# Optimization experiments

Measured on AMD Instinct MI355X. Metric: run time of the kernel, lower is better.

The kernel has to match this reference:

```python
import jax, jax.numpy as jnp
import numpy as np

B, N, D, L = 8, 128, 512, 48
NUM_GCN_LAYERS = 2


def setup_inputs() -> dict:
    key = jax.random.key(0)
    ks = jax.random.split(key, 10)
    gcn_inputs = jax.random.normal(ks[0], (B, N, D), dtype=jnp.float32)
    word_seq_len = jax.random.randint(ks[1], (B,), 1, N + 1)
    adj_matrix = jax.random.randint(ks[2], (B, N, N), 0, 2).astype(jnp.float32)
    dep_label_matrix = jax.random.randint(ks[3], (B, N, N), 0, L)
    # per-label weight matrices, stored (L, out_dim, in_dim) as consumed by the bmm
    w_params = jax.random.normal(ks[4], (L, D, D), dtype=jnp.float32) * 0.05
    mlp_w0 = jax.random.normal(ks[5], (D, D), dtype=jnp.float32) * (1.0 / np.sqrt(D))
    mlp_b0 = jnp.zeros((D,), dtype=jnp.float32)
    mlp_w1 = jax.random.normal(ks[6], (D, D), dtype=jnp.float32) * (1.0 / np.sqrt(D))
    mlp_b1 = jnp.zeros((D,), dtype=jnp.float32)
    return {
        'gcn_inputs': gcn_inputs,
        'word_seq_len': word_seq_len,
        'adj_matrix': adj_matrix,
        'dep_label_matrix': dep_label_matrix,
        'w_params': w_params,
        'mlp_w0': mlp_w0,
        'mlp_b0': mlp_b0,
        'mlp_w1': mlp_w1,
        'mlp_b1': mlp_b1,
    }


def reference(gcn_inputs, word_seq_len, adj_matrix, dep_label_matrix,
              w_params, mlp_w0, mlp_b0, mlp_w1, mlp_b1):
    # denom: in-degree + 1 (self)
    denom = adj_matrix.sum(axis=2, keepdims=True) + 1.0  # (B, N, 1)
    b_idx = jnp.arange(B)[:, None, None]                  # (B,1,1)
    j_idx = jnp.arange(N)[None, None, :]                  # (1,1,N)
    h = gcn_inputs
    for _ in range(NUM_GCN_LAYERS):
        # transform every node by every label matrix: (B, L, N, D)
        t = jnp.einsum('ldk,bjk->bljd', w_params, h)
        # gather per-edge label transform: g[b,i,j,:] = t[b, lab[b,i,j], j, :]
        g = t[b_idx, dep_label_matrix, j_idx]             # (B, N, N, D)
        msg = (adj_matrix[..., None] * g).sum(axis=2)     # (B, N, D)
        h = jax.nn.relu(msg / denom)
    x = jax.nn.relu(h @ mlp_w0.T + mlp_b0)
    x = jax.nn.relu(x @ mlp_w1.T + mlp_b1)
    return x
```

## Files before the change

kernel.cpp:

```cpp
#include <hip/hip_runtime.h>
#include <hip/hip_bf16.h>


typedef unsigned short u16;
typedef unsigned int u32;
using bf16x8 = __bf16 __attribute__((ext_vector_type(8)));
using f32x4 = float __attribute__((ext_vector_type(4)));

__device__ __forceinline__ u16 f2bf(float f) {
  u32 u = __float_as_uint(f);
  u32 r = u + 0x7fffu + ((u >> 16) & 1u);
  return (u16)(r >> 16);
}
__device__ __forceinline__ float bf2f(u16 h) {
  return __uint_as_float(((u32)h) << 16);
}

__device__ __forceinline__ void gl_lds16(const u16* g, u16* l) {
  __builtin_amdgcn_global_load_lds(
      (const __attribute__((address_space(1))) u32*)g,
      (__attribute__((address_space(3))) u32*)l, 16, 0, 0);
}

__global__ __launch_bounds__(256)
void cvt_f32_bf16(const float* __restrict__ in, u16* __restrict__ out, int n4) {
  int stride = gridDim.x * blockDim.x;
  for (int i = blockIdx.x * blockDim.x + threadIdx.x; i < n4; i += stride) {
    float4 v = ((const float4*)in)[i];
    uint2 o;
    o.x = (u32)f2bf(v.x) | ((u32)f2bf(v.y) << 16);
    o.y = (u32)f2bf(v.z) | ((u32)f2bf(v.w) << 16);
    ((uint2*)out)[i] = o;
  }
}

__global__ __launch_bounds__(256)
void prep_mlp_w(const float* __restrict__ w0, const float* __restrict__ w1,
                u16* __restrict__ Bp1, u16* __restrict__ Bp2) {
  int idx = blockIdx.x * 256 + threadIdx.x;
  if (idx < 262144) {
    const int n = idx >> 9, k = idx & 511;
    const float v = w0[idx];
    const u16 hi = f2bf(v);
    const float lo = v - bf2f(hi);
    Bp1[n * 1024 + k] = hi;
    Bp1[n * 1024 + 512 + k] = f2bf(lo);
  } else {
    const int j = idx - 262144;
    const int n = j >> 9, k = j & 511;
    const float v = w1[j];
    const u16 hi = f2bf(v);
    const float lo = v - bf2f(hi);
    Bp2[n * 1536 + k] = hi;
    Bp2[n * 1536 + 512 + k] = f2bf(lo);
    Bp2[n * 1536 + 1024 + k] = hi;
  }
}

#define BM 128
#define BN 128
#define BK 32

template <int MODE>
__global__ __launch_bounds__(256)
void gemm_nt_bf16(const u16* __restrict__ A, const u16* __restrict__ B,
                  void* __restrict__ C, int N, int K, int KC) {
  __shared__ u16 sA[3][BM * BK];
  __shared__ u16 sB[3][BN * BK];
  const int tid = threadIdx.x;
  const int lane = tid & 63;
  const int wid = tid >> 6;
  const int wm = wid >> 1;
  const int wn = wid & 1;

  int m0, n0, kc;
  if (MODE == 0) {
    const int bid = blockIdx.x;
    const int xcd = bid & 7;
    const int r = bid >> 3;
    m0 = (r & 7) * BM;
    n0 = (xcd * 24 + (r >> 3)) * BN;
    kc = 0;
  } else {
    m0 = blockIdx.y * BM;
    n0 = blockIdx.x * BN;
    kc = blockIdx.z;
  }

  const int srow = tid >> 2;
  const int scol = (tid & 3) * 8;
  const u16* gA0 = A + (size_t)(m0 + srow) * K + kc * KC + scol;
  const u16* gA1 = A + (size_t)(m0 + 64 + srow) * K + kc * KC + scol;
  const u16* gB0 = B + (size_t)(n0 + srow) * K + kc * KC + scol;
  const u16* gB1 = B + (size_t)(n0 + 64 + srow) * K + kc * KC + scol;

  auto stage = [&](int buf, int kt) {
    const int ko = kt * BK;
    gl_lds16(gA0 + ko, &sA[buf][tid * 8]);
    gl_lds16(gA1 + ko, &sA[buf][2048 + tid * 8]);
    gl_lds16(gB0 + ko, &sB[buf][tid * 8]);
    gl_lds16(gB1 + ko, &sB[buf][2048 + tid * 8]);
  };

  f32x4 acc[4][4];
#pragma unroll
  for (int i = 0; i < 4; ++i)
#pragma unroll
    for (int j = 0; j < 4; ++j)
      acc[i][j] = (f32x4){0.f, 0.f, 0.f, 0.f};

  const int NT = KC / BK;

  stage(0, 0);
  if (NT > 1) {
    stage(1, 1);
    asm volatile("s_waitcnt vmcnt(4)" ::: "memory");
  } else {
    asm volatile("s_waitcnt vmcnt(0)" ::: "memory");
  }
  __builtin_amdgcn_s_barrier();
  __builtin_amdgcn_sched_barrier(0);

  const int r15 = lane & 15;
  const int ksub = (lane >> 4) * 8;
  for (int kt = 0; kt < NT; ++kt) {
    const int buf = kt % 3;
    if (kt + 2 < NT) stage((kt + 2) % 3, kt + 2);

    bf16x8 af[4], bfr[4];
#pragma unroll
    for (int mi = 0; mi < 4; ++mi)
      af[mi] = *(const bf16x8*)&sA[buf][(wm * 64 + mi * 16 + r15) * BK + ksub];
#pragma unroll
    for (int ni = 0; ni < 4; ++ni)
      bfr[ni] = *(const bf16x8*)&sB[buf][(wn * 64 + ni * 16 + r15) * BK + ksub];

#pragma unroll
    for (int mi = 0; mi < 4; ++mi)
#pragma unroll
      for (int ni = 0; ni < 4; ++ni)
        acc[mi][ni] = __builtin_amdgcn_mfma_f32_16x16x32_bf16(
            af[mi], bfr[ni], acc[mi][ni], 0, 0, 0);

    if (kt + 1 < NT) {
      if (kt + 2 < NT)
        asm volatile("s_waitcnt vmcnt(4)" ::: "memory");
      else
        asm volatile("s_waitcnt vmcnt(0)" ::: "memory");
      __builtin_amdgcn_s_barrier();
      __builtin_amdgcn_sched_barrier(0);
    }
  }

  const int rq = (lane >> 4) * 4;
#pragma unroll
  for (int mi = 0; mi < 4; ++mi) {
#pragma unroll
    for (int ni = 0; ni < 4; ++ni) {
      const int row = m0 + wm * 64 + mi * 16 + rq;
      const int col = n0 + wn * 64 + ni * 16 + r15;
      f32x4 v = acc[mi][ni];
      if (MODE == 0) {
        u16* Cb = (u16*)C;
        const size_t base = (size_t)row * N + col;
#pragma unroll
        for (int r = 0; r < 4; ++r)
          Cb[base + (size_t)r * N] = f2bf(v[r]);
      } else {
        float* Cf = (float*)C + (size_t)kc * 1024 * N;
#pragma unroll
        for (int r = 0; r < 4; ++r)
          Cf[(size_t)(row + r) * N + col] = v[r];
      }
    }
  }
}

template <bool DUP>
__global__ __launch_bounds__(256)
void gcn_agg(const u16* __restrict__ T, const float* __restrict__ adj,
             const int* __restrict__ lab, u16* __restrict__ Hout) {
  const int bid = blockIdx.x;
  const int b = bid & 7;
  const int i = bid >> 3;
  const int bi = b * 128 + i;
  const int tid = threadIdx.x;
  __shared__ float s_adj[128];
  __shared__ int s_off[128];
  if (tid < 128) {
    s_adj[tid] = adj[(size_t)bi * 128 + tid];
    const int lv = lab[(size_t)bi * 128 + tid];
    s_off[tid] = ((b * 128 + tid) * 48 + lv) * 512;
  }
  __syncthreads();

  const int d = tid * 2;
  float den = 1.0f, a0 = 0.f, a1 = 0.f;
#pragma unroll 4
  for (int j = 0; j < 128; ++j) {
    const float a = s_adj[j];
    if (a != 0.0f) {
      den += 1.0f;
      const u32 u = *(const u32*)&T[(size_t)s_off[j] + d];
      a0 += __uint_as_float((u & 0xffffu) << 16);
      a1 += __uint_as_float(u & 0xffff0000u);
    }
  }
  const float r = 1.0f / den;
  a0 = fmaxf(a0 * r, 0.0f);
  a1 = fmaxf(a1 * r, 0.0f);
  const u32 o = (u32)f2bf(a0) | ((u32)f2bf(a1) << 16);
  if (DUP) {
    *(u32*)&Hout[(size_t)bi * 1024 + d] = o;
    *(u32*)&Hout[(size_t)bi * 1024 + 512 + d] = o;
  } else {
    *(u32*)&Hout[(size_t)bi * 512 + d] = o;
  }
}

__global__ __launch_bounds__(256)
void combine_mlp1(const float* __restrict__ P, const float* __restrict__ bias,
                  u16* __restrict__ Ap2) {
  const int idx = blockIdx.x * 256 + threadIdx.x;
  const int m = idx >> 8;
  const int n = (idx & 255) * 2;
  float s0 = 0.f, s1 = 0.f;
#pragma unroll
  for (int s = 0; s < 4; ++s) {
    const float2 v = *(const float2*)&P[(size_t)s * 524288 + m * 512 + n];
    s0 += v.x; s1 += v.y;
  }
  const float x0 = fmaxf(s0 + bias[n], 0.f);
  const float x1 = fmaxf(s1 + bias[n + 1], 0.f);
  const u16 h0 = f2bf(x0), h1 = f2bf(x1);
  const float l0 = x0 - bf2f(h0), l1 = x1 - bf2f(h1);
  const u32 hh = (u32)h0 | ((u32)h1 << 16);
  const u32 ll = (u32)f2bf(l0) | ((u32)f2bf(l1) << 16);
  const size_t base = (size_t)m * 1536 + n;
  *(u32*)&Ap2[base] = hh;
  *(u32*)&Ap2[base + 512] = hh;
  *(u32*)&Ap2[base + 1024] = ll;
}

__global__ __launch_bounds__(256)
void combine_mlp2(const float* __restrict__ P, const float* __restrict__ bias,
                  float* __restrict__ out) {
  const int idx = blockIdx.x * 256 + threadIdx.x;
  const int m = idx >> 7;
  const int n = (idx & 127) * 4;
  float4 s = {0.f, 0.f, 0.f, 0.f};
#pragma unroll
  for (int t = 0; t < 6; ++t) {
    const float4 v = *(const float4*)&P[(size_t)t * 524288 + m * 512 + n];
    s.x += v.x; s.y += v.y; s.z += v.z; s.w += v.w;
  }
  const float4 b = *(const float4*)&bias[n];
  float4 o;
  o.x = fmaxf(s.x + b.x, 0.f);
  o.y = fmaxf(s.y + b.y, 0.f);
  o.z = fmaxf(s.z + b.z, 0.f);
  o.w = fmaxf(s.w + b.w, 0.f);
  *(float4*)&out[(size_t)m * 512 + n] = o;
}

extern "C" void kernel_launch(void* const* d_in, const int* in_sizes, int n_in,
                              void* d_out, int out_size, void* d_ws, size_t ws_size,
                              hipStream_t stream) {
  const float* gcn_inputs = (const float*)d_in[0];
  const float* adj = (const float*)d_in[2];
  const int* lab = (const int*)d_in[3];
  const float* w_params = (const float*)d_in[4];
  const float* w0 = (const float*)d_in[5];
  const float* b0 = (const float*)d_in[6];
  const float* w1 = (const float*)d_in[7];
  const float* b1 = (const float*)d_in[8];
  float* out = (float*)d_out;

  char* ws = (char*)d_ws;
  u16* Wbf = (u16*)ws;
  float* P = (float*)ws;
  u16* T = (u16*)(ws + 25165824);
  u16* Bp1 = T;
  u16* Bp2 = (u16*)(ws + 25165824 + (1 << 20));
  u16* Ha = (u16*)(ws + 75497472);
  u16* Hb = (u16*)(ws + 76546048);
  u16* Ap1 = (u16*)(ws + 77594624);
  u16* Ap2 = (u16*)(ws + 79691776);

  cvt_f32_bf16<<<2048, 256, 0, stream>>>(w_params, Wbf, (48 * 512 * 512) / 4);
  cvt_f32_bf16<<<512, 256, 0, stream>>>(gcn_inputs, Ha, (8 * 128 * 512) / 4);

  gemm_nt_bf16<0><<<1536, 256, 0, stream>>>(Ha, Wbf, T, 24576, 512, 512);
  gcn_agg<false><<<1024, 256, 0, stream>>>(T, adj, lab, Hb);
  gemm_nt_bf16<0><<<1536, 256, 0, stream>>>(Hb, Wbf, T, 24576, 512, 512);
  gcn_agg<true><<<1024, 256, 0, stream>>>(T, adj, lab, Ap1);

  prep_mlp_w<<<2048, 256, 0, stream>>>(w0, w1, Bp1, Bp2);

  dim3 g1(512 / BN, 1024 / BM, 4);
  gemm_nt_bf16<1><<<g1, 256, 0, stream>>>(Ap1, Bp1, P, 512, 1024, 256);
  combine_mlp1<<<1024, 256, 0, stream>>>(P, b0, Ap2);
  dim3 g2(512 / BN, 1024 / BM, 6);
  gemm_nt_bf16<1><<<g2, 256, 0, stream>>>(Ap2, Bp2, P, 512, 1536, 256);
  combine_mlp2<<<512, 256, 0, stream>>>(P, b1, out);
}
```

Measured before the change: 175.9 us.

## Swizzle GEMM LDS layout, fuse conversion kernels, deepen split-K for MLP GEMMs

Applies an XOR swizzle to the LDS tile column layout in the bf16 GEMM to reduce bank conflicts on fragment reads. It also sets a minimum-occupancy launch bound, merges the two f32-to-bf16 conversion launches into one kernel, and doubles the split-K factor for the MLP GEMMs with matching reductions in the combine kernels. These changes target LDS conflicts, launch overhead and low block counts in the small MLP GEMMs. In exchange they write more partial-sum traffic and may add register pressure.

```diff
diff --git a/kernel.cpp b/kernel.cpp
--- a/kernel.cpp
+++ b/kernel.cpp
@@ -23,14 +23,25 @@
 }
 
 __global__ __launch_bounds__(256)
-void cvt_f32_bf16(const float* __restrict__ in, u16* __restrict__ out, int n4) {
-  int stride = gridDim.x * blockDim.x;
-  for (int i = blockIdx.x * blockDim.x + threadIdx.x; i < n4; i += stride) {
-    float4 v = ((const float4*)in)[i];
+void cvt_all(const float* __restrict__ w_in, u16* __restrict__ w_out,
+             const float* __restrict__ h_in, u16* __restrict__ h_out) {
+  if (blockIdx.x < 2048) {
+    const int n4 = (48 * 512 * 512) / 4;
+    const int stride = 2048 * 256;
+    for (int i = blockIdx.x * 256 + threadIdx.x; i < n4; i += stride) {
+      float4 v = ((const float4*)w_in)[i];
+      uint2 o;
+      o.x = (u32)f2bf(v.x) | ((u32)f2bf(v.y) << 16);
+      o.y = (u32)f2bf(v.z) | ((u32)f2bf(v.w) << 16);
+      ((uint2*)w_out)[i] = o;
+    }
+  } else {
+    const int i = (blockIdx.x - 2048) * 256 + threadIdx.x;
+    float4 v = ((const float4*)h_in)[i];
     uint2 o;
     o.x = (u32)f2bf(v.x) | ((u32)f2bf(v.y) << 16);
     o.y = (u32)f2bf(v.z) | ((u32)f2bf(v.w) << 16);
-    ((uint2*)out)[i] = o;
+    ((uint2*)h_out)[i] = o;
   }
 }
 
@@ -62,7 +73,7 @@
 #define BK 32
 
 template <int MODE>
-__global__ __launch_bounds__(256)
+__global__ __launch_bounds__(256, 3)
 void gemm_nt_bf16(const u16* __restrict__ A, const u16* __restrict__ B,
                   void* __restrict__ C, int N, int K, int KC) {
   __shared__ u16 sA[3][BM * BK];
@@ -88,7 +99,7 @@
   }
 
   const int srow = tid >> 2;
-  const int scol = (tid & 3) * 8;
+  const int scol = ((tid & 3) ^ ((tid >> 3) & 3)) * 8;
   const u16* gA0 = A + (size_t)(m0 + srow) * K + kc * KC + scol;
   const u16* gA1 = A + (size_t)(m0 + 64 + srow) * K + kc * KC + scol;
   const u16* gB0 = B + (size_t)(n0 + srow) * K + kc * KC + scol;
@@ -122,7 +133,7 @@
   __builtin_amdgcn_sched_barrier(0);
 
   const int r15 = lane & 15;
-  const int ksub = (lane >> 4) * 8;
+  const int colswz = (((lane >> 4) ^ ((r15 >> 1) & 3))) * 8;
   for (int kt = 0; kt < NT; ++kt) {
     const int buf = kt % 3;
     if (kt + 2 < NT) stage((kt + 2) % 3, kt + 2);
@@ -130,10 +141,10 @@
     bf16x8 af[4], bfr[4];
 #pragma unroll
     for (int mi = 0; mi < 4; ++mi)
-      af[mi] = *(const bf16x8*)&sA[buf][(wm * 64 + mi * 16 + r15) * BK + ksub];
+      af[mi] = *(const bf16x8*)&sA[buf][(wm * 64 + mi * 16 + r15) * BK + colswz];
 #pragma unroll
     for (int ni = 0; ni < 4; ++ni)
-      bfr[ni] = *(const bf16x8*)&sB[buf][(wn * 64 + ni * 16 + r15) * BK + ksub];
+      bfr[ni] = *(const bf16x8*)&sB[buf][(wn * 64 + ni * 16 + r15) * BK + colswz];
 
 #pragma unroll
     for (int mi = 0; mi < 4; ++mi)
@@ -226,7 +237,7 @@
   const int n = (idx & 255) * 2;
   float s0 = 0.f, s1 = 0.f;
 #pragma unroll
-  for (int s = 0; s < 4; ++s) {
+  for (int s = 0; s < 8; ++s) {
     const float2 v = *(const float2*)&P[(size_t)s * 524288 + m * 512 + n];
     s0 += v.x; s1 += v.y;
   }
@@ -250,7 +261,7 @@
   const int n = (idx & 127) * 4;
   float4 s = {0.f, 0.f, 0.f, 0.f};
 #pragma unroll
-  for (int t = 0; t < 6; ++t) {
+  for (int t = 0; t < 12; ++t) {
     const float4 v = *(const float4*)&P[(size_t)t * 524288 + m * 512 + n];
     s.x += v.x; s.y += v.y; s.z += v.z; s.w += v.w;
   }
@@ -287,8 +298,7 @@
   u16* Ap1 = (u16*)(ws + 77594624);
   u16* Ap2 = (u16*)(ws + 79691776);
 
-  cvt_f32_bf16<<<2048, 256, 0, stream>>>(w_params, Wbf, (48 * 512 * 512) / 4);
-  cvt_f32_bf16<<<512, 256, 0, stream>>>(gcn_inputs, Ha, (8 * 128 * 512) / 4);
+  cvt_all<<<2560, 256, 0, stream>>>(w_params, Wbf, gcn_inputs, Ha);
 
   gemm_nt_bf16<0><<<1536, 256, 0, stream>>>(Ha, Wbf, T, 24576, 512, 512);
   gcn_agg<false><<<1024, 256, 0, stream>>>(T, adj, lab, Hb);
@@ -297,10 +307,10 @@
 
   prep_mlp_w<<<2048, 256, 0, stream>>>(w0, w1, Bp1, Bp2);
 
-  dim3 g1(512 / BN, 1024 / BM, 4);
-  gemm_nt_bf16<1><<<g1, 256, 0, stream>>>(Ap1, Bp1, P, 512, 1024, 256);
+  dim3 g1(512 / BN, 1024 / BM, 8);
+  gemm_nt_bf16<1><<<g1, 256, 0, stream>>>(Ap1, Bp1, P, 512, 1024, 128);
   combine_mlp1<<<1024, 256, 0, stream>>>(P, b0, Ap2);
-  dim3 g2(512 / BN, 1024 / BM, 6);
-  gemm_nt_bf16<1><<<g2, 256, 0, stream>>>(Ap2, Bp2, P, 512, 1536, 256);
+  dim3 g2(512 / BN, 1024 / BM, 12);
+  gemm_nt_bf16<1><<<g2, 256, 0, stream>>>(Ap2, Bp2, P, 512, 1536, 128);
   combine_mlp2<<<512, 256, 0, stream>>>(P, b1, out);
 }
```

Result: no change. 175.3 us (-0.3%).
